# Kernel optimization log

Hardware: AMD Instinct MI355X
Metric: run time of the kernel (lower is better)

## Reference

```python
import jax, jax.numpy as jnp
import numpy as np

N_SETS, N_POINTS, D_FEAT = 8, 4096, 16
K = 16


def setup_inputs() -> dict:
    key = jax.random.key(0)
    x = jax.random.normal(key, (N_SETS, N_POINTS, D_FEAT), dtype=jnp.float32)
    return {"x": x, "k": K}


def reference(x, k):
    """Faithful kNN-graph construction.

    x: (N, M, D) point sets. Returns (src, dst) flattened edge lists with
    per-sample node-ID offsets (node j of set i -> global id i*M + j), plus
    the top-k squared distances (the selection values).
    """
    n_samples, n_points, _ = x.shape
    # pairwise squared distance: ||xi||^2 + ||xj||^2 - 2 xi.xj  -> (N, M, M)
    x2s = jnp.sum(x * x, axis=-1, keepdims=True)
    dist = x2s + jnp.swapaxes(x2s, -1, -2) - 2.0 * jnp.einsum("nmd,npd->nmp", x, x)
    # k smallest distances per row (argtopk descending=False)
    neg_vals, k_indices = jax.lax.top_k(-dist, k)            # (N, M, k)
    topk_dist = -neg_vals
    per_sample_offset = (jnp.arange(n_samples, dtype=jnp.int32) * n_points)[:, None, None]
    dst = k_indices.astype(jnp.int32) + per_sample_offset     # neighbor ids
    src = jnp.broadcast_to(
        jnp.arange(n_points, dtype=jnp.int32)[None, :, None], k_indices.shape
    ) + per_sample_offset                                     # query ids
    return src.reshape(-1), dst.reshape(-1), topk_dist
```

## Files before the change

kernel.cpp:

```cpp
#include <hip/hip_runtime.h>
#include <hip/hip_bf16.h>

#define NSETS 8
#define NPTS  4096
#define DF    16
#define KNN   16
#define QPB   64
#define NCH   8
#define BLK   (QPB * NCH)
#define TILE  512
#define NTILE (NPTS / TILE)
#define SLICE (TILE / NCH)
#define NEDGE (NSETS * NPTS * KNN)

#define RES      8
#define FLUSH_AT 5
#define GRP      4

#define FEAT_B   (TILE * DF * 4)
#define NRM_B    (TILE * 4)
#define RESV_OFF (FEAT_B + NRM_B)
#define SMEM_B   (RESV_OFF + RES * BLK * 8)

__global__ __launch_bounds__(BLK) void knn_kernel(const float* __restrict__ x,
                                                  float* __restrict__ out) {
    __shared__ float tau_sh[QPB];
    __shared__ __align__(16) char smem[SMEM_B];
    float4* feat4 = (float4*)smem;
    float*  nrm_t = (float*)(smem + FEAT_B);
    float2* resv  = (float2*)(smem + RESV_OFF);
    float*          lds_d = (float*)smem;
    unsigned short* lds_i = (unsigned short*)(smem + BLK * KNN * 4);

    const int t    = threadIdx.x;
    const int lane = t & 63;
    const int wv   = t >> 6;
    const int set  = blockIdx.x >> 6;
    const int q0   = (blockIdx.x & 63) * QPB;
    const int q    = q0 + lane;

    const float* xs = x + (size_t)set * NPTS * DF;

    if (t < QPB) tau_sh[t] = 3.0e38f;

    float qn[DF];
    float q2;
    {
        const float4* qp = (const float4*)(xs + (size_t)q * DF);
        float4 a = qp[0], b = qp[1], g = qp[2], d = qp[3];
        float r0 = __fadd_rn(__fmul_rn(a.x, a.x), __fmul_rn(g.x, g.x));
        float r1 = __fadd_rn(__fmul_rn(a.y, a.y), __fmul_rn(g.y, g.y));
        float r2 = __fadd_rn(__fmul_rn(a.z, a.z), __fmul_rn(g.z, g.z));
        float r3 = __fadd_rn(__fmul_rn(a.w, a.w), __fmul_rn(g.w, g.w));
        float r4 = __fadd_rn(__fmul_rn(b.x, b.x), __fmul_rn(d.x, d.x));
        float r5 = __fadd_rn(__fmul_rn(b.y, b.y), __fmul_rn(d.y, d.y));
        float r6 = __fadd_rn(__fmul_rn(b.z, b.z), __fmul_rn(d.z, d.z));
        float r7 = __fadd_rn(__fmul_rn(b.w, b.w), __fmul_rn(d.w, d.w));
        q2 = __fadd_rn(__fadd_rn(__fadd_rn(r0, r1), __fadd_rn(r2, r3)),
                       __fadd_rn(__fadd_rn(r4, r5), __fadd_rn(r6, r7)));
        qn[0]=a.x; qn[1]=a.y; qn[2]=a.z; qn[3]=a.w;
        qn[4]=b.x; qn[5]=b.y; qn[6]=b.z; qn[7]=b.w;
        qn[8]=g.x; qn[9]=g.y; qn[10]=g.z; qn[11]=g.w;
        qn[12]=d.x; qn[13]=d.y; qn[14]=d.z; qn[15]=d.w;
#pragma unroll
        for (int d2 = 0; d2 < DF; ++d2) qn[d2] = -2.0f * qn[d2];
    }

    float Ld[KNN];
    int   Li[KNN];
#pragma unroll
    for (int j = 0; j < KNN; ++j) { Ld[j] = 3.0e38f; Li[j] = 0; }
    int cnt = 0;

    auto flush = [&]() {
        for (int e = 0; e < RES; ++e) {
            if (!__any(e < cnt)) break;
            float2 en = resv[e * BLK + t];
            const float d  = (e < cnt) ? en.x : 3.0e38f;
            const int   ci = __float_as_int(en.y);
            if (d < Ld[KNN - 1]) {
#pragma unroll
                for (int j = KNN - 1; j >= 1; --j) {
                    const bool sh   = d < Ld[j - 1];
                    const bool here = d < Ld[j];
                    const float nd = sh ? Ld[j - 1] : (here ? d  : Ld[j]);
                    const int   ni = sh ? Li[j - 1] : (here ? ci : Li[j]);
                    Ld[j] = nd; Li[j] = ni;
                }
                if (d < Ld[0]) { Ld[0] = d; Li[0] = ci; }
            }
        }
        cnt = 0;
        volatile float* ts = (volatile float*)tau_sh;
        float cur = ts[lane];
        ts[lane] = fminf(cur, Ld[KNN - 1]);
    };

    for (int tile = 0; tile < NTILE; ++tile) {
        __syncthreads();
        {
            const int c = tile * TILE + t;
            const float4* p = (const float4*)(xs + (size_t)c * DF);
            float4 a = p[0], b = p[1], g = p[2], d = p[3];
            float r0 = __fadd_rn(__fmul_rn(a.x, a.x), __fmul_rn(g.x, g.x));
            float r1 = __fadd_rn(__fmul_rn(a.y, a.y), __fmul_rn(g.y, g.y));
            float r2 = __fadd_rn(__fmul_rn(a.z, a.z), __fmul_rn(g.z, g.z));
            float r3 = __fadd_rn(__fmul_rn(a.w, a.w), __fmul_rn(g.w, g.w));
            float r4 = __fadd_rn(__fmul_rn(b.x, b.x), __fmul_rn(d.x, d.x));
            float r5 = __fadd_rn(__fmul_rn(b.y, b.y), __fmul_rn(d.y, d.y));
            float r6 = __fadd_rn(__fmul_rn(b.z, b.z), __fmul_rn(d.z, d.z));
            float r7 = __fadd_rn(__fmul_rn(b.w, b.w), __fmul_rn(d.w, d.w));
            feat4[0 * TILE + t] = a;
            feat4[1 * TILE + t] = b;
            feat4[2 * TILE + t] = g;
            feat4[3 * TILE + t] = d;
            nrm_t[t] = __fadd_rn(
                __fadd_rn(__fadd_rn(r0, r1), __fadd_rn(r2, r3)),
                __fadd_rn(__fadd_rn(r4, r5), __fadd_rn(r6, r7)));
        }
        __syncthreads();

        const int lbase = wv * SLICE;
        const int gbase = tile * TILE + lbase;

        for (int g = 0; g < SLICE; g += GRP) {
            const float tsh = ((volatile float*)tau_sh)[lane];
            const float tau = fminf(tsh, Ld[KNN - 1]);
#pragma unroll
            for (int u = 0; u < GRP; ++u) {
                const int lc = lbase + g + u;
                float4 f0 = feat4[0 * TILE + lc];
                float4 f1 = feat4[1 * TILE + lc];
                float4 f2 = feat4[2 * TILE + lc];
                float4 f3 = feat4[3 * TILE + lc];
                const float nc = nrm_t[lc];
                float dot = 0.f;
                dot = fmaf(qn[0],  f0.x, dot); dot = fmaf(qn[1],  f0.y, dot);
                dot = fmaf(qn[2],  f0.z, dot); dot = fmaf(qn[3],  f0.w, dot);
                dot = fmaf(qn[4],  f1.x, dot); dot = fmaf(qn[5],  f1.y, dot);
                dot = fmaf(qn[6],  f1.z, dot); dot = fmaf(qn[7],  f1.w, dot);
                dot = fmaf(qn[8],  f2.x, dot); dot = fmaf(qn[9],  f2.y, dot);
                dot = fmaf(qn[10], f2.z, dot); dot = fmaf(qn[11], f2.w, dot);
                dot = fmaf(qn[12], f3.x, dot); dot = fmaf(qn[13], f3.y, dot);
                dot = fmaf(qn[14], f3.z, dot); dot = fmaf(qn[15], f3.w, dot);
                const float dist = __fadd_rn(__fadd_rn(q2, nc), dot);
                if (dist <= tau) {
                    resv[cnt * BLK + t] =
                        make_float2(dist, __int_as_float(gbase + g + u));
                    ++cnt;
                }
            }
            if (__any(cnt >= FLUSH_AT)) flush();
        }
    }
    flush();

    __syncthreads();
#pragma unroll
    for (int j = 0; j < KNN; ++j) {
        lds_d[t * KNN + j] = Ld[j];
        lds_i[t * KNN + j] = (unsigned short)Li[j];
    }
    __syncthreads();

    if (t < QPB) {
        const int l = t;
        float h[NCH];
        int   hi[NCH];
        int   p[NCH];
#pragma unroll
        for (int w2 = 0; w2 < NCH; ++w2) {
            p[w2]  = 0;
            h[w2]  = lds_d[(w2 * QPB + l) * KNN];
            hi[w2] = (int)lds_i[(w2 * QPB + l) * KNN];
        }

        const int    gq = set * NPTS + q0 + l;
        const size_t eb = (size_t)gq * KNN;
        float* osrc = out;
        float* odst = out + (size_t)NEDGE;
        float* odis = out + 2 * (size_t)NEDGE;
        const float srcf = (float)gq;

        for (int e = 0; e < KNN; ++e) {
            float best = h[0];
            int   bi   = hi[0];
            int   bw   = 0;
#pragma unroll
            for (int w2 = 1; w2 < NCH; ++w2) {
                const bool better = (h[w2] < best) ||
                                    (h[w2] == best && hi[w2] < bi);
                if (better) { best = h[w2]; bi = hi[w2]; bw = w2; }
            }

#pragma unroll
            for (int w2 = 0; w2 < NCH; ++w2) {
                if (bw == w2) {
                    ++p[w2];
                    if (p[w2] < KNN) {
                        h[w2]  = lds_d[(w2 * QPB + l) * KNN + p[w2]];
                        hi[w2] = (int)lds_i[(w2 * QPB + l) * KNN + p[w2]];
                    } else {
                        h[w2]  = 3.0e38f;
                        hi[w2] = 0x7FFFFFFF;
                    }
                }
            }

            osrc[eb + e] = srcf;
            odst[eb + e] = (float)(set * NPTS + bi);
            odis[eb + e] = best;
        }
    }
}

extern "C" void kernel_launch(void* const* d_in, const int* in_sizes, int n_in,
                              void* d_out, int out_size, void* d_ws, size_t ws_size,
                              hipStream_t stream) {
    (void)in_sizes; (void)n_in; (void)out_size; (void)d_ws; (void)ws_size;
    const float* x = (const float*)d_in[0];
    float* out = (float*)d_out;

    knn_kernel<<<NSETS * (NPTS / QPB), BLK, 0, stream>>>(x, out);
}
```

Before: 229.2 us.

## Process two queries per thread to reuse shared-memory candidate loads

Each thread now keeps two query points, each with its own running top-16 list, and scores every candidate feature read from shared memory against both. This halves the shared-memory feature traffic per distance and raises arithmetic intensity. In exchange, the grid shrinks to half as many blocks, per-thread register pressure roughly doubles, and the reservoir buffers and shared memory grow. Both lists are flushed whenever either fills, so some flushes run early.

Result: slower. 392.1 us (+71.1%).

```diff
diff --git a/kernel.cpp b/kernel.cpp
--- a/kernel.cpp
+++ b/kernel.cpp
@@ -5,48 +5,52 @@
 #define NPTS  4096
 #define DF    16
 #define KNN   16
-#define QPB   64
-#define NCH   8
-#define BLK   (QPB * NCH)
+#define QG    2
+#define QPB   (64 * QG)
+#define NWV   8
+#define BLK   512
 #define TILE  512
 #define NTILE (NPTS / TILE)
-#define SLICE (TILE / NCH)
+#define WSLICE (TILE / NWV)
 #define NEDGE (NSETS * NPTS * KNN)
 
-#define RES      8
-#define FLUSH_AT 5
+#define RES      12
+#define FLUSH_AT 9
 #define GRP      4
 
 #define FEAT_B   (TILE * DF * 4)
 #define NRM_B    (TILE * 4)
 #define RESV_OFF (FEAT_B + NRM_B)
-#define SMEM_B   (RESV_OFF + RES * BLK * 8)
-
-__global__ __launch_bounds__(BLK) void knn_kernel(const float* __restrict__ x,
-                                                  float* __restrict__ out) {
+#define RESV_B   (QG * RES * BLK * 8)
+#define SMEM_B   (RESV_OFF + RESV_B)
+
+__global__ __launch_bounds__(BLK, 2) void knn_kernel(const float* __restrict__ x,
+                                                     float* __restrict__ out) {
     __shared__ float tau_sh[QPB];
     __shared__ __align__(16) char smem[SMEM_B];
     float4* feat4 = (float4*)smem;
     float*  nrm_t = (float*)(smem + FEAT_B);
-    float2* resv  = (float2*)(smem + RESV_OFF);
+    float2* resvA = (float2*)(smem + RESV_OFF);
+    float2* resvB = resvA + RES * BLK;
     float*          lds_d = (float*)smem;
-    unsigned short* lds_i = (unsigned short*)(smem + BLK * KNN * 4);
+    unsigned short* lds_i = (unsigned short*)(smem + QG * BLK * KNN * 4);
 
     const int t    = threadIdx.x;
     const int lane = t & 63;
     const int wv   = t >> 6;
-    const int set  = blockIdx.x >> 6;
-    const int q0   = (blockIdx.x & 63) * QPB;
-    const int q    = q0 + lane;
+    const int set  = blockIdx.x >> 5;
+    const int q0   = (blockIdx.x & 31) * QPB;
+    const int qa   = q0 + lane;
+    const int qb   = q0 + 64 + lane;
 
     const float* xs = x + (size_t)set * NPTS * DF;
 
     if (t < QPB) tau_sh[t] = 3.0e38f;
 
-    float qn[DF];
-    float q2;
+    float qnA[DF], qnB[DF];
+    float q2A, q2B;
     {
-        const float4* qp = (const float4*)(xs + (size_t)q * DF);
+        const float4* qp = (const float4*)(xs + (size_t)qa * DF);
         float4 a = qp[0], b = qp[1], g = qp[2], d = qp[3];
         float r0 = __fadd_rn(__fmul_rn(a.x, a.x), __fmul_rn(g.x, g.x));
         float r1 = __fadd_rn(__fmul_rn(a.y, a.y), __fmul_rn(g.y, g.y));
@@ -56,26 +60,47 @@
         float r5 = __fadd_rn(__fmul_rn(b.y, b.y), __fmul_rn(d.y, d.y));
         float r6 = __fadd_rn(__fmul_rn(b.z, b.z), __fmul_rn(d.z, d.z));
         float r7 = __fadd_rn(__fmul_rn(b.w, b.w), __fmul_rn(d.w, d.w));
-        q2 = __fadd_rn(__fadd_rn(__fadd_rn(r0, r1), __fadd_rn(r2, r3)),
-                       __fadd_rn(__fadd_rn(r4, r5), __fadd_rn(r6, r7)));
-        qn[0]=a.x; qn[1]=a.y; qn[2]=a.z; qn[3]=a.w;
-        qn[4]=b.x; qn[5]=b.y; qn[6]=b.z; qn[7]=b.w;
-        qn[8]=g.x; qn[9]=g.y; qn[10]=g.z; qn[11]=g.w;
-        qn[12]=d.x; qn[13]=d.y; qn[14]=d.z; qn[15]=d.w;
-#pragma unroll
-        for (int d2 = 0; d2 < DF; ++d2) qn[d2] = -2.0f * qn[d2];
-    }
-
-    float Ld[KNN];
-    int   Li[KNN];
-#pragma unroll
-    for (int j = 0; j < KNN; ++j) { Ld[j] = 3.0e38f; Li[j] = 0; }
-    int cnt = 0;
-
-    auto flush = [&]() {
+        q2A = __fadd_rn(__fadd_rn(__fadd_rn(r0, r1), __fadd_rn(r2, r3)),
+                        __fadd_rn(__fadd_rn(r4, r5), __fadd_rn(r6, r7)));
+        qnA[0]=a.x; qnA[1]=a.y; qnA[2]=a.z; qnA[3]=a.w;
+        qnA[4]=b.x; qnA[5]=b.y; qnA[6]=b.z; qnA[7]=b.w;
+        qnA[8]=g.x; qnA[9]=g.y; qnA[10]=g.z; qnA[11]=g.w;
+        qnA[12]=d.x; qnA[13]=d.y; qnA[14]=d.z; qnA[15]=d.w;
+    }
+    {
+        const float4* qp = (const float4*)(xs + (size_t)qb * DF);
+        float4 a = qp[0], b = qp[1], g = qp[2], d = qp[3];
+        float r0 = __fadd_rn(__fmul_rn(a.x, a.x), __fmul_rn(g.x, g.x));
+        float r1 = __fadd_rn(__fmul_rn(a.y, a.y), __fmul_rn(g.y, g.y));
+        float r2 = __fadd_rn(__fmul_rn(a.z, a.z), __fmul_rn(g.z, g.z));
+        float r3 = __fadd_rn(__fmul_rn(a.w, a.w), __fmul_rn(g.w, g.w));
+        float r4 = __fadd_rn(__fmul_rn(b.x, b.x), __fmul_rn(d.x, d.x));
+        float r5 = __fadd_rn(__fmul_rn(b.y, b.y), __fmul_rn(d.y, d.y));
+        float r6 = __fadd_rn(__fmul_rn(b.z, b.z), __fmul_rn(d.z, d.z));
+        float r7 = __fadd_rn(__fmul_rn(b.w, b.w), __fmul_rn(d.w, d.w));
+        q2B = __fadd_rn(__fadd_rn(__fadd_rn(r0, r1), __fadd_rn(r2, r3)),
+                        __fadd_rn(__fadd_rn(r4, r5), __fadd_rn(r6, r7)));
+        qnB[0]=a.x; qnB[1]=a.y; qnB[2]=a.z; qnB[3]=a.w;
+        qnB[4]=b.x; qnB[5]=b.y; qnB[6]=b.z; qnB[7]=b.w;
+        qnB[8]=g.x; qnB[9]=g.y; qnB[10]=g.z; qnB[11]=g.w;
+        qnB[12]=d.x; qnB[13]=d.y; qnB[14]=d.z; qnB[15]=d.w;
+    }
+#pragma unroll
+    for (int d2 = 0; d2 < DF; ++d2) { qnA[d2] = -2.0f * qnA[d2];
+                                      qnB[d2] = -2.0f * qnB[d2]; }
+
+    float LdA[KNN], LdB[KNN];
+    int   LiA[KNN], LiB[KNN];
+#pragma unroll
+    for (int j = 0; j < KNN; ++j) { LdA[j] = 3.0e38f; LiA[j] = 0;
+                                    LdB[j] = 3.0e38f; LiB[j] = 0; }
+    int cntA = 0, cntB = 0;
+
+    auto flush1 = [&](float2* rb, float (&Ld)[KNN], int (&Li)[KNN],
+                      int& cnt, int tidx) {
         for (int e = 0; e < RES; ++e) {
             if (!__any(e < cnt)) break;
-            float2 en = resv[e * BLK + t];
+            float2 en = rb[e * BLK + t];
             const float d  = (e < cnt) ? en.x : 3.0e38f;
             const int   ci = __float_as_int(en.y);
             if (d < Ld[KNN - 1]) {
@@ -92,8 +117,8 @@
         }
         cnt = 0;
         volatile float* ts = (volatile float*)tau_sh;
-        float cur = ts[lane];
-        ts[lane] = fminf(cur, Ld[KNN - 1]);
+        float cur = ts[tidx];
+        ts[tidx] = fminf(cur, Ld[KNN - 1]);
     };
 
     for (int tile = 0; tile < NTILE; ++tile) {
@@ -120,12 +145,14 @@
         }
         __syncthreads();
 
-        const int lbase = wv * SLICE;
+        const int lbase = wv * WSLICE;
         const int gbase = tile * TILE + lbase;
 
-        for (int g = 0; g < SLICE; g += GRP) {
-            const float tsh = ((volatile float*)tau_sh)[lane];
-            const float tau = fminf(tsh, Ld[KNN - 1]);
+        for (int g = 0; g < WSLICE; g += GRP) {
+            const float tA = fminf(((volatile float*)tau_sh)[lane],
+                                   LdA[KNN - 1]);
+            const float tB = fminf(((volatile float*)tau_sh)[64 + lane],
+                                   LdB[KNN - 1]);
 #pragma unroll
             for (int u = 0; u < GRP; ++u) {
                 const int lc = lbase + g + u;
@@ -134,45 +161,69 @@
                 float4 f2 = feat4[2 * TILE + lc];
                 float4 f3 = feat4[3 * TILE + lc];
                 const float nc = nrm_t[lc];
-                float dot = 0.f;
-                dot = fmaf(qn[0],  f0.x, dot); dot = fmaf(qn[1],  f0.y, dot);
-                dot = fmaf(qn[2],  f0.z, dot); dot = fmaf(qn[3],  f0.w, dot);
-                dot = fmaf(qn[4],  f1.x, dot); dot = fmaf(qn[5],  f1.y, dot);
-                dot = fmaf(qn[6],  f1.z, dot); dot = fmaf(qn[7],  f1.w, dot);
-                dot = fmaf(qn[8],  f2.x, dot); dot = fmaf(qn[9],  f2.y, dot);
-                dot = fmaf(qn[10], f2.z, dot); dot = fmaf(qn[11], f2.w, dot);
-                dot = fmaf(qn[12], f3.x, dot); dot = fmaf(qn[13], f3.y, dot);
-                dot = fmaf(qn[14], f3.z, dot); dot = fmaf(qn[15], f3.w, dot);
-                const float dist = __fadd_rn(__fadd_rn(q2, nc), dot);
-                if (dist <= tau) {
-                    resv[cnt * BLK + t] =
-                        make_float2(dist, __int_as_float(gbase + g + u));
-                    ++cnt;
-                }
-            }
-            if (__any(cnt >= FLUSH_AT)) flush();
-        }
-    }
-    flush();
+                float dA = 0.f, dB = 0.f;
+                dA = fmaf(qnA[0],  f0.x, dA); dB = fmaf(qnB[0],  f0.x, dB);
+                dA = fmaf(qnA[1],  f0.y, dA); dB = fmaf(qnB[1],  f0.y, dB);
+                dA = fmaf(qnA[2],  f0.z, dA); dB = fmaf(qnB[2],  f0.z, dB);
+                dA = fmaf(qnA[3],  f0.w, dA); dB = fmaf(qnB[3],  f0.w, dB);
+                dA = fmaf(qnA[4],  f1.x, dA); dB = fmaf(qnB[4],  f1.x, dB);
+                dA = fmaf(qnA[5],  f1.y, dA); dB = fmaf(qnB[5],  f1.y, dB);
+                dA = fmaf(qnA[6],  f1.z, dA); dB = fmaf(qnB[6],  f1.z, dB);
+                dA = fmaf(qnA[7],  f1.w, dA); dB = fmaf(qnB[7],  f1.w, dB);
+                dA = fmaf(qnA[8],  f2.x, dA); dB = fmaf(qnB[8],  f2.x, dB);
+                dA = fmaf(qnA[9],  f2.y, dA); dB = fmaf(qnB[9],  f2.y, dB);
+                dA = fmaf(qnA[10], f2.z, dA); dB = fmaf(qnB[10], f2.z, dB);
+                dA = fmaf(qnA[11], f2.w, dA); dB = fmaf(qnB[11], f2.w, dB);
+                dA = fmaf(qnA[12], f3.x, dA); dB = fmaf(qnB[12], f3.x, dB);
+                dA = fmaf(qnA[13], f3.y, dA); dB = fmaf(qnB[13], f3.y, dB);
+                dA = fmaf(qnA[14], f3.z, dA); dB = fmaf(qnB[14], f3.z, dB);
+                dA = fmaf(qnA[15], f3.w, dA); dB = fmaf(qnB[15], f3.w, dB);
+                const float distA = __fadd_rn(__fadd_rn(q2A, nc), dA);
+                const float distB = __fadd_rn(__fadd_rn(q2B, nc), dB);
+                const int ci = gbase + g + u;
+                if (distA <= tA) {
+                    resvA[cntA * BLK + t] = make_float2(distA, __int_as_float(ci));
+                    ++cntA;
+                }
+                if (distB <= tB) {
+                    resvB[cntB * BLK + t] = make_float2(distB, __int_as_float(ci));
+                    ++cntB;
+                }
+            }
+            if (__any((cntA >= FLUSH_AT) || (cntB >= FLUSH_AT))) {
+                flush1(resvA, LdA, LiA, cntA, lane);
+                flush1(resvB, LdB, LiB, cntB, 64 + lane);
+            }
+        }
+    }
+    flush1(resvA, LdA, LiA, cntA, lane);
+    flush1(resvB, LdB, LiB, cntB, 64 + lane);
 
     __syncthreads();
 #pragma unroll
     for (int j = 0; j < KNN; ++j) {
-        lds_d[t * KNN + j] = Ld[j];
-        lds_i[t * KNN + j] = (unsigned short)Li[j];
+        lds_d[t * KNN + j] = LdA[j];
+        lds_d[BLK * KNN + t * KNN + j] = LdB[j];
+        lds_i[t * KNN + j] = (unsigned short)LiA[j];
+        lds_i[BLK * KNN + t * KNN + j] = (unsigned short)LiB[j];
     }
     __syncthreads();
 
     if (t < QPB) {
-        const int l = t;
-        float h[NCH];
-        int   hi[NCH];
-        int   p[NCH];
-#pragma unroll
-        for (int w2 = 0; w2 < NCH; ++w2) {
+        const int l    = t;
+        const int grp  = l >> 6;
+        const int ln   = l & 63;
+        const int gofs = grp * BLK * KNN;
+
+        float h[NWV];
+        int   hi[NWV];
+        int   p[NWV];
+#pragma unroll
+        for (int w2 = 0; w2 < NWV; ++w2) {
+            const int base = gofs + (w2 * 64 + ln) * KNN;
             p[w2]  = 0;
-            h[w2]  = lds_d[(w2 * QPB + l) * KNN];
-            hi[w2] = (int)lds_i[(w2 * QPB + l) * KNN];
+            h[w2]  = lds_d[base];
+            hi[w2] = (int)lds_i[base];
         }
 
         const int    gq = set * NPTS + q0 + l;
@@ -187,19 +238,20 @@
             int   bi   = hi[0];
             int   bw   = 0;
 #pragma unroll
-            for (int w2 = 1; w2 < NCH; ++w2) {
+            for (int w2 = 1; w2 < NWV; ++w2) {
                 const bool better = (h[w2] < best) ||
                                     (h[w2] == best && hi[w2] < bi);
                 if (better) { best = h[w2]; bi = hi[w2]; bw = w2; }
             }
 
 #pragma unroll
-            for (int w2 = 0; w2 < NCH; ++w2) {
+            for (int w2 = 0; w2 < NWV; ++w2) {
                 if (bw == w2) {
                     ++p[w2];
+                    const int base = gofs + (w2 * 64 + ln) * KNN;
                     if (p[w2] < KNN) {
-                        h[w2]  = lds_d[(w2 * QPB + l) * KNN + p[w2]];
-                        hi[w2] = (int)lds_i[(w2 * QPB + l) * KNN + p[w2]];
+                        h[w2]  = lds_d[base + p[w2]];
+                        hi[w2] = (int)lds_i[base + p[w2]];
                     } else {
                         h[w2]  = 3.0e38f;
                         hi[w2] = 0x7FFFFFFF;
```
